# Kernel optimization log

Hardware: AMD Instinct MI355X
Metric: run time of the kernel (lower is better)

Reference implementation:

```python
import jax, jax.numpy as jnp
import numpy as np

B, T, OBS, H, A, S = 4096, 64, 64, 64, 8, 201


def setup_inputs() -> dict:
    key = jax.random.key(0)
    ks = jax.random.split(key, 13)
    n = lambda k, shp, s=1.0: jax.random.normal(k, shp, dtype=jnp.float32) * s
    return {
        "x": n(ks[0], (B, T, OBS)),
        "stack": jnp.zeros((B, S, H), jnp.float32),
        "stack_ptrs": jax.random.randint(ks[1], (B, 1), 0, 100, dtype=jnp.int32),
        # core_network: init.normal_(std=1.0) per source
        "W1": n(ks[2], (H, OBS + H)), "b1": n(ks[3], (H,)),
        "W2": n(ks[4], (H, H)), "b2": n(ks[5], (H,)),
        # stack_head: default torch Linear init ~ U(-1/sqrt(H), 1/sqrt(H))
        "Ws": (jax.random.uniform(ks[6], (3, H), dtype=jnp.float32) * 2 - 1) / np.sqrt(H),
        "bs": (jax.random.uniform(ks[7], (3,), dtype=jnp.float32) * 2 - 1) / np.sqrt(H),
        # policy/value heads: init.normal_(std=0.01)
        "Wp": n(ks[8], (A, H), 0.01), "bp": n(ks[9], (A,), 0.01),
        "Wv": n(ks[10], (1, H), 0.01), "bv": n(ks[11], (1,), 0.01),
    }


def reference(x, stack, stack_ptrs, W1, b1, W2, b2, Ws, bs, Wp, bp, Wv, bv):
    # x: [B,T,OBS]  stack: [B,S,H]  stack_ptrs: [B,1] int
    batch = x.shape[0]
    bidx = jnp.arange(batch)
    ptrs0 = stack_ptrs.astype(jnp.int32)[:, 0]  # [B]

    def step(carry, x_t):
        stk, ptrs = carry
        top = stk[bidx, ptrs]                                   # [B,H] gather at ptr
        h = jnp.tanh(jnp.concatenate([x_t, top], axis=1) @ W1.T + b1)
        p = jnp.tanh(h @ W2.T + b2)                             # [B,H]
        probs = jax.nn.softmax(p @ Ws.T + bs, axis=1)           # [B,3]
        ops = jnp.argmax(probs, axis=1).astype(jnp.int32)       # 0=pop,1=noop,2=push
        push = (ops == 2)[:, None]
        # conditional scatter: write p at row ptr only where op==2
        stk = stk.at[bidx, ptrs].set(jnp.where(push, p, top))
        ptrs = jnp.maximum(ptrs + ops - 1, 0)
        logits = p @ Wp.T + bp                                  # [B,A]
        value = (p @ Wv.T + bv)[:, 0]                           # [B]
        return (stk, ptrs), (logits, value)

    (stack_out, ptrs_out), (logits_t, values_t) = jax.lax.scan(
        step, (stack, ptrs0), jnp.swapaxes(x, 0, 1))
    logitss = jnp.swapaxes(logits_t, 0, 1)      # [B,T,A]
    values = values_t.reshape(-1)               # time-major [T*B], matching torch layout
    return logitss, values, stack_out, ptrs_out[:, None]
```

## Files before the change

### kernel.cpp

```cpp
#include <hip/hip_runtime.h>
#include <cstddef>

#define NB 4096
#define NT 64
#define NOBS 64
#define NH 64
#define NA 8
#define NS 201


__global__ void copy_stack_kernel(const float4* __restrict__ src,
                                  float4* __restrict__ dst, int n4) {
    int i = blockIdx.x * blockDim.x + threadIdx.x;
    if (i < n4) dst[i] = src[i];
}

__launch_bounds__(256, 2)
__global__ void stacknet_kernel(const float* __restrict__ x,
                                const int* __restrict__ ptrs_in,
                                const float* __restrict__ W1,
                                const float* __restrict__ b1,
                                const float* __restrict__ W2,
                                const float* __restrict__ b2,
                                const float* __restrict__ Ws,
                                const float* __restrict__ bs,
                                const float* __restrict__ Wp,
                                const float* __restrict__ bp,
                                const float* __restrict__ Wv,
                                const float* __restrict__ bv,
                                float* __restrict__ logits_out,
                                float* __restrict__ values_out,
                                float* __restrict__ stack,
                                float* __restrict__ ptrs_out) {
    const int lane = threadIdx.x & 63;
    const int wv = threadIdx.x >> 6;
    const int b = (blockIdx.x << 2) + wv;
    const int aa = lane & 15;

    __shared__ __align__(16) float shw[16 * 68];
    __shared__ float shb[16];
    __shared__ __align__(16) float vbuf[4][256];

    for (int i = threadIdx.x; i < 16 * 64; i += 256) {
        int a = i >> 6, k = i & 63;
        float w = 0.0f;
        if (a < 3)        w = Ws[a * 64 + k];
        else if (a < 11)  w = Wp[(a - 3) * 64 + k];
        else if (a == 11) w = Wv[k];
        shw[a * 68 + k] = w;
    }
    if (threadIdx.x < 16) {
        int a = threadIdx.x;
        float bb = 0.0f;
        if (a < 3) bb = bs[a];
        else if (a < 11) bb = bp[a - 3];
        else if (a == 11) bb = bv[0];
        shb[a] = bb;
    }
    __syncthreads();

    float w1r[128];
#pragma unroll
    for (int j = 0; j < 32; ++j) {
        float4 tW = ((const float4*)W1)[lane * 32 + j];
        w1r[4*j] = tW.x; w1r[4*j+1] = tW.y; w1r[4*j+2] = tW.z; w1r[4*j+3] = tW.w;
    }
    float w2r[64];
#pragma unroll
    for (int j = 0; j < 16; ++j) {
        float4 tW = ((const float4*)W2)[lane * 16 + j];
        w2r[4*j] = tW.x; w2r[4*j+1] = tW.y; w2r[4*j+2] = tW.z; w2r[4*j+3] = tW.w;
    }
    float b1r = b1[lane];
    float b2r = b2[lane];

    int ptr = ptrs_in[b];
    const float* xb  = x + (size_t)b * NT * NOBS;
    float* stk       = stack + (size_t)b * NS * NH;
    float* lgb       = logits_out + (size_t)b * NT * NA;

    float* v = &vbuf[wv][0];
    const float* shwa = &shw[aa * 68];
    const float shba = shb[aa];

    float top = stk[ptr * 64 + lane];
    bool pushed = false;
    float pushval = 0.0f;

    for (int t = 0; t < NT; ++t) {
        int r0 = (ptr > 0) ? (ptr - 1) : 0;
        float c0 = stk[r0 * 64 + lane];
        float c2 = stk[(ptr + 1) * 64 + lane];
        float xv = xb[t * 64 + lane];

        v[lane]      = xv;
        v[64 + lane] = top;

        float acc = 0.0f;
        const float4* v4 = (const float4*)v;
#pragma unroll
        for (int j = 0; j < 32; ++j) {
            float4 a4 = v4[j];
            acc = fmaf(w1r[4*j],   a4.x, acc);
            acc = fmaf(w1r[4*j+1], a4.y, acc);
            acc = fmaf(w1r[4*j+2], a4.z, acc);
            acc = fmaf(w1r[4*j+3], a4.w, acc);
        }
        float h = tanhf(acc + b1r);
        v[128 + lane] = h;

        float acc2 = 0.0f;
        const float4* h4 = (const float4*)(v + 128);
#pragma unroll
        for (int j = 0; j < 16; ++j) {
            float4 a4 = h4[j];
            acc2 = fmaf(w2r[4*j],   a4.x, acc2);
            acc2 = fmaf(w2r[4*j+1], a4.y, acc2);
            acc2 = fmaf(w2r[4*j+2], a4.z, acc2);
            acc2 = fmaf(w2r[4*j+3], a4.w, acc2);
        }
        float p = tanhf(acc2 + b2r);
        v[192 + lane] = p;

        float hacc = 0.0f;
        const float4* p4 = (const float4*)(v + 192);
#pragma unroll
        for (int j = 0; j < 16; ++j) {
            float4 w4 = *(const float4*)(shwa + 4*j);
            float4 a4 = p4[j];
            hacc = fmaf(a4.x, w4.x, hacc);
            hacc = fmaf(a4.y, w4.y, hacc);
            hacc = fmaf(a4.z, w4.z, hacc);
            hacc = fmaf(a4.w, w4.w, hacc);
        }
        float sv = hacc + shba;

        float s0 = __shfl(sv, 0, 64), s1 = __shfl(sv, 1, 64), s2 = __shfl(sv, 2, 64);
        float m = fmaxf(fmaxf(s0, s1), s2);
        float e0 = expf(s0 - m), e1 = expf(s1 - m), e2 = expf(s2 - m);
        float S = (e0 + e1) + e2;
        float p0 = e0 / S, p1 = e1 / S, p2 = e2 / S;
        int op = 0; float pm = p0;
        if (p1 > pm) { pm = p1; op = 1; }
        if (p2 > pm) { op = 2; }

        if (op == 2) stk[ptr * 64 + lane] = p;

        float sel = (op == 0) ? (pushed ? pushval : c0)
                              : ((op == 1) ? top : c2);
        pushed = (op == 2);
        pushval = p;

        int np = ptr + op - 1;
        ptr = (np < 0) ? 0 : np;
        top = sel;

        if (lane >= 3 && lane <= 10) {
            lgb[t * NA + (lane - 3)] = sv;
        }
        if (lane == 11) {
            values_out[(size_t)t * NB + b] = sv;
        }
    }
    if (lane == 0) ptrs_out[b] = (float)ptr;
}

extern "C" void kernel_launch(void* const* d_in, const int* in_sizes, int n_in,
                              void* d_out, int out_size, void* d_ws, size_t ws_size,
                              hipStream_t stream) {
    const float* x        = (const float*)d_in[0];
    const float* stack_in = (const float*)d_in[1];
    const int*   ptrs_in  = (const int*)d_in[2];
    const float* W1 = (const float*)d_in[3];
    const float* b1 = (const float*)d_in[4];
    const float* W2 = (const float*)d_in[5];
    const float* b2 = (const float*)d_in[6];
    const float* Ws = (const float*)d_in[7];
    const float* bs = (const float*)d_in[8];
    const float* Wp = (const float*)d_in[9];
    const float* bp = (const float*)d_in[10];
    const float* Wv = (const float*)d_in[11];
    const float* bv = (const float*)d_in[12];

    float* out      = (float*)d_out;
    float* logits   = out;
    float* values   = out + 2097152;
    float* stack    = out + 2359296;
    float* ptrs_out = out + 55050240;

    int n4 = 52690944 / 4;
    copy_stack_kernel<<<51456, 256, 0, stream>>>((const float4*)stack_in,
                                                 (float4*)stack, n4);
    stacknet_kernel<<<1024, 256, 0, stream>>>(x, ptrs_in, W1, b1, W2, b2,
                                              Ws, bs, Wp, bp, Wv, bv,
                                              logits, values, stack, ptrs_out);
}
```

Baseline: 745.1 us.

## Fuse stack copy into recurrent kernel, precompute input projection, use readlane broadcasts

Removes the separate stack-copy kernel: each wave now copies its own batch's stack slice before running the recurrence. The x-part of the first layer is precomputed for all timesteps into shared memory, so the sequential loop only does the hidden-state half. Matrix-vector products now broadcast activations with readlane instead of going through an LDS buffer, and all head weights are kept in registers. Blocks shrink to 2 waves, and a two-entry cache of recently pushed rows replaces the single pushed flag. The costs are high register pressure and roughly 32 KB of shared memory per block, which may limit occupancy.

Result: slower. 933.2 us (+25.3%).

```diff
diff --git a/kernel.cpp b/kernel.cpp
--- a/kernel.cpp
+++ b/kernel.cpp
@@ -9,14 +9,13 @@
 #define NS 201
 
 
-__global__ void copy_stack_kernel(const float4* __restrict__ src,
-                                  float4* __restrict__ dst, int n4) {
-    int i = blockIdx.x * blockDim.x + threadIdx.x;
-    if (i < n4) dst[i] = src[i];
+__device__ __forceinline__ float bl(float v, int k) {
+    return __int_as_float(__builtin_amdgcn_readlane(__float_as_int(v), k));
 }
 
-__launch_bounds__(256, 2)
+__launch_bounds__(128, 2)
 __global__ void stacknet_kernel(const float* __restrict__ x,
+                                const float* __restrict__ stack_in,
                                 const int* __restrict__ ptrs_in,
                                 const float* __restrict__ W1,
                                 const float* __restrict__ b1,
@@ -33,134 +32,129 @@
                                 float* __restrict__ stack,
                                 float* __restrict__ ptrs_out) {
     const int lane = threadIdx.x & 63;
-    const int wv = threadIdx.x >> 6;
-    const int b = (blockIdx.x << 2) + wv;
-    const int aa = lane & 15;
+    const int wv   = threadIdx.x >> 6;
+    const int b    = (blockIdx.x << 1) + wv;
+    const int aa   = lane & 15;
 
-    __shared__ __align__(16) float shw[16 * 68];
-    __shared__ float shb[16];
-    __shared__ __align__(16) float vbuf[4][256];
+    __shared__ __align__(16) float xcl[2][NT * NH];
 
-    for (int i = threadIdx.x; i < 16 * 64; i += 256) {
-        int a = i >> 6, k = i & 63;
-        float w = 0.0f;
-        if (a < 3)        w = Ws[a * 64 + k];
-        else if (a < 11)  w = Wp[(a - 3) * 64 + k];
-        else if (a == 11) w = Wv[k];
-        shw[a * 68 + k] = w;
+    const float* xb = x + (size_t)b * NT * NOBS;
+    float* stk      = stack + (size_t)b * NS * NH;
+
+    {
+        const float4* s4 = (const float4*)(stack_in + (size_t)b * (NS * NH));
+        float4* d4 = (float4*)stk;
+#pragma unroll 4
+        for (int i = lane; i < (NS * NH / 4); i += 64) d4[i] = s4[i];
     }
-    if (threadIdx.x < 16) {
-        int a = threadIdx.x;
-        float bb = 0.0f;
-        if (a < 3) bb = bs[a];
-        else if (a < 11) bb = bp[a - 3];
-        else if (a == 11) bb = bv[0];
-        shb[a] = bb;
+
+    {
+        float w1x[64];
+#pragma unroll
+        for (int j = 0; j < 16; ++j) {
+            float4 w = ((const float4*)W1)[lane * 32 + j];
+            w1x[4*j] = w.x; w1x[4*j+1] = w.y; w1x[4*j+2] = w.z; w1x[4*j+3] = w.w;
+        }
+        float* xcw = xcl[wv];
+        float xv = xb[lane];
+#pragma unroll 1
+        for (int t = 0; t < NT; ++t) {
+            float xnext = (t + 1 < NT) ? xb[(t + 1) * 64 + lane] : 0.f;
+            float acc = 0.f;
+#pragma unroll
+            for (int k = 0; k < 64; ++k) acc = fmaf(w1x[k], bl(xv, k), acc);
+            xcw[t * 64 + lane] = acc;
+            xv = xnext;
+        }
     }
-    __syncthreads();
 
-    float w1r[128];
-#pragma unroll
-    for (int j = 0; j < 32; ++j) {
-        float4 tW = ((const float4*)W1)[lane * 32 + j];
-        w1r[4*j] = tW.x; w1r[4*j+1] = tW.y; w1r[4*j+2] = tW.z; w1r[4*j+3] = tW.w;
-    }
-    float w2r[64];
+    float w1h[64], w2r[64], hw[64];
 #pragma unroll
     for (int j = 0; j < 16; ++j) {
-        float4 tW = ((const float4*)W2)[lane * 16 + j];
-        w2r[4*j] = tW.x; w2r[4*j+1] = tW.y; w2r[4*j+2] = tW.z; w2r[4*j+3] = tW.w;
+        float4 wa = ((const float4*)W1)[lane * 32 + 16 + j];
+        w1h[4*j] = wa.x; w1h[4*j+1] = wa.y; w1h[4*j+2] = wa.z; w1h[4*j+3] = wa.w;
+        float4 wb = ((const float4*)W2)[lane * 16 + j];
+        w2r[4*j] = wb.x; w2r[4*j+1] = wb.y; w2r[4*j+2] = wb.z; w2r[4*j+3] = wb.w;
     }
-    float b1r = b1[lane];
-    float b2r = b2[lane];
-
-    int ptr = ptrs_in[b];
-    const float* xb  = x + (size_t)b * NT * NOBS;
-    float* stk       = stack + (size_t)b * NS * NH;
-    float* lgb       = logits_out + (size_t)b * NT * NA;
-
-    float* v = &vbuf[wv][0];
-    const float* shwa = &shw[aa * 68];
-    const float shba = shb[aa];
-
-    float top = stk[ptr * 64 + lane];
-    bool pushed = false;
-    float pushval = 0.0f;
-
-    for (int t = 0; t < NT; ++t) {
-        int r0 = (ptr > 0) ? (ptr - 1) : 0;
-        float c0 = stk[r0 * 64 + lane];
-        float c2 = stk[(ptr + 1) * 64 + lane];
-        float xv = xb[t * 64 + lane];
-
-        v[lane]      = xv;
-        v[64 + lane] = top;
-
-        float acc = 0.0f;
-        const float4* v4 = (const float4*)v;
-#pragma unroll
-        for (int j = 0; j < 32; ++j) {
-            float4 a4 = v4[j];
-            acc = fmaf(w1r[4*j],   a4.x, acc);
-            acc = fmaf(w1r[4*j+1], a4.y, acc);
-            acc = fmaf(w1r[4*j+2], a4.z, acc);
-            acc = fmaf(w1r[4*j+3], a4.w, acc);
-        }
-        float h = tanhf(acc + b1r);
-        v[128 + lane] = h;
-
-        float acc2 = 0.0f;
-        const float4* h4 = (const float4*)(v + 128);
+    if (aa < 12) {
+        const float* hsrc = (aa < 3) ? (Ws + aa * 64)
+                          : (aa < 11) ? (Wp + (aa - 3) * 64) : Wv;
 #pragma unroll
         for (int j = 0; j < 16; ++j) {
-            float4 a4 = h4[j];
-            acc2 = fmaf(w2r[4*j],   a4.x, acc2);
-            acc2 = fmaf(w2r[4*j+1], a4.y, acc2);
-            acc2 = fmaf(w2r[4*j+2], a4.z, acc2);
-            acc2 = fmaf(w2r[4*j+3], a4.w, acc2);
+            float4 w = *(const float4*)(hsrc + 4 * j);
+            hw[4*j] = w.x; hw[4*j+1] = w.y; hw[4*j+2] = w.z; hw[4*j+3] = w.w;
         }
+    } else {
+#pragma unroll
+        for (int k = 0; k < 64; ++k) hw[k] = 0.f;
+    }
+    float b1r  = b1[lane];
+    float b2r  = b2[lane];
+    float shba = (aa < 3) ? bs[aa] : (aa < 11) ? bp[aa - 3] : (aa == 11) ? bv[0] : 0.f;
+
+    asm volatile("s_waitcnt vmcnt(0)" ::: "memory");
+
+    int ptr   = ptrs_in[b];
+    float top = stk[ptr * 64 + lane];
+    int   lastRow = -1, lastRow2 = -1;
+    float lastVal = 0.f, lastVal2 = 0.f;
+
+    const float* xcw = xcl[wv];
+    float* lgb = logits_out + (size_t)b * NT * NA;
+
+#pragma unroll 1
+    for (int t = 0; t < NT; ++t) {
+        int r0    = (ptr > 0) ? (ptr - 1) : 0;
+        float c0  = stk[r0 * 64 + lane];
+        float c2  = stk[(ptr + 1) * 64 + lane];
+        float xcv = xcw[t * 64 + lane];
+
+        float acc = xcv;
+#pragma unroll
+        for (int k = 0; k < 64; ++k) acc = fmaf(w1h[k], bl(top, k), acc);
+        float h = tanhf(acc + b1r);
+
+        float acc2 = 0.f;
+#pragma unroll
+        for (int k = 0; k < 64; ++k) acc2 = fmaf(w2r[k], bl(h, k), acc2);
         float p = tanhf(acc2 + b2r);
-        v[192 + lane] = p;
 
-        float hacc = 0.0f;
-        const float4* p4 = (const float4*)(v + 192);
+        float hacc = 0.f;
 #pragma unroll
-        for (int j = 0; j < 16; ++j) {
-            float4 w4 = *(const float4*)(shwa + 4*j);
-            float4 a4 = p4[j];
-            hacc = fmaf(a4.x, w4.x, hacc);
-            hacc = fmaf(a4.y, w4.y, hacc);
-            hacc = fmaf(a4.z, w4.z, hacc);
-            hacc = fmaf(a4.w, w4.w, hacc);
-        }
+        for (int k = 0; k < 64; ++k) hacc = fmaf(hw[k], bl(p, k), hacc);
         float sv = hacc + shba;
 
-        float s0 = __shfl(sv, 0, 64), s1 = __shfl(sv, 1, 64), s2 = __shfl(sv, 2, 64);
-        float m = fmaxf(fmaxf(s0, s1), s2);
-        float e0 = expf(s0 - m), e1 = expf(s1 - m), e2 = expf(s2 - m);
+        float s0 = bl(sv, 0), s1 = bl(sv, 1), s2 = bl(sv, 2);
+        float mx = fmaxf(fmaxf(s0, s1), s2);
+        float e0 = expf(s0 - mx), e1 = expf(s1 - mx), e2 = expf(s2 - mx);
         float S = (e0 + e1) + e2;
-        float p0 = e0 / S, p1 = e1 / S, p2 = e2 / S;
-        int op = 0; float pm = p0;
-        if (p1 > pm) { pm = p1; op = 1; }
-        if (p2 > pm) { op = 2; }
+        float q0 = e0 / S, q1 = e1 / S, q2 = e2 / S;
+        int op = 0; float pm = q0;
+        if (q1 > pm) { pm = q1; op = 1; }
+        if (q2 > pm) { op = 2; }
 
         if (op == 2) stk[ptr * 64 + lane] = p;
 
-        float sel = (op == 0) ? (pushed ? pushval : c0)
-                              : ((op == 1) ? top : c2);
-        pushed = (op == 2);
-        pushval = p;
+        float sel;
+        if (op == 0) {
+            sel = (r0 == lastRow) ? lastVal
+                : (r0 == lastRow2) ? lastVal2 : c0;
+        } else if (op == 1) {
+            sel = top;
+        } else {
+            int r2 = ptr + 1;
+            sel = (r2 == lastRow) ? lastVal
+                : (r2 == lastRow2) ? lastVal2 : c2;
+        }
+        if (op == 2) { lastRow2 = lastRow; lastVal2 = lastVal;
+                       lastRow = ptr;      lastVal  = p; }
 
         int np = ptr + op - 1;
         ptr = (np < 0) ? 0 : np;
         top = sel;
 
-        if (lane >= 3 && lane <= 10) {
-            lgb[t * NA + (lane - 3)] = sv;
-        }
-        if (lane == 11) {
-            values_out[(size_t)t * NB + b] = sv;
-        }
+        if (lane >= 3 && lane <= 10) lgb[t * NA + (lane - 3)] = sv;
+        if (lane == 11) values_out[(size_t)t * NB + b] = sv;
     }
     if (lane == 0) ptrs_out[b] = (float)ptr;
 }
@@ -188,10 +182,8 @@
     float* stack    = out + 2359296;
     float* ptrs_out = out + 55050240;
 
-    int n4 = 52690944 / 4;
-    copy_stack_kernel<<<51456, 256, 0, stream>>>((const float4*)stack_in,
-                                                 (float4*)stack, n4);
-    stacknet_kernel<<<1024, 256, 0, stream>>>(x, ptrs_in, W1, b1, W2, b2,
-                                              Ws, bs, Wp, bp, Wv, bv,
-                                              logits, values, stack, ptrs_out);
+    stacknet_kernel<<<NB / 2, 128, 0, stream>>>(x, stack_in, ptrs_in,
+                                                W1, b1, W2, b2, Ws, bs,
+                                                Wp, bp, Wv, bv,
+                                                logits, values, stack, ptrs_out);
 }
```
